# Kernel optimization log

Hardware: AMD Instinct MI355X
Metric: run time of the kernel (lower is better)

## Reference

```python
import jax, jax.numpy as jnp
import numpy as np

NINP = 512
NHEAD = 8


def setup_inputs() -> dict:
    key = jax.random.key(0)
    ks = jax.random.split(key, 7)
    B, M, L, C = 2, 32, 512, NINP
    s = 1.0 / np.sqrt(C)
    return {
        "x": jax.random.normal(ks[0], (B, M, L, C), dtype=jnp.float32),
        "Wq": jax.random.normal(ks[1], (C, C), dtype=jnp.float32) * s,
        "bq": jax.random.normal(ks[2], (C,), dtype=jnp.float32) * s,
        "Wk": jax.random.normal(ks[3], (C, C), dtype=jnp.float32) * s,
        "bk": jax.random.normal(ks[4], (C,), dtype=jnp.float32) * s,
        "Wv": jax.random.normal(ks[5], (C, C), dtype=jnp.float32) * s,
        "bv": jax.random.normal(ks[6], (C,), dtype=jnp.float32) * s,
    }


def reference(x, Wq, bq, Wk, bk, Wv, bv) -> jnp.ndarray:
    # x: (B, M, L, C). Attention over L within each (B, M) block.
    B, M, L, C = x.shape
    H = NHEAD
    D = C // H
    scale = 1.0 / jnp.sqrt(jnp.asarray(D, dtype=x.dtype))

    def split_heads(t):  # (B,M,L,C) -> (B,M,H,L,D)
        return t.reshape(B, M, L, H, D).transpose(0, 1, 3, 2, 4)

    q = split_heads(x @ Wq + bq)
    k = split_heads(x @ Wk + bk)
    v = split_heads(x @ Wv + bv)

    scores = jnp.einsum("bmhid,bmhjd->bmhij", q, k) * scale
    w = jax.nn.softmax(scores, axis=-1)  # dropout p=0 -> identity
    out = jnp.einsum("bmhij,bmhjd->bmhid", w, v)  # (B,M,H,L,D)
    return out.transpose(0, 1, 3, 2, 4).reshape(B, M, L, C)
```

## Files before the change

kernel.cpp:

```cpp
#include <hip/hip_runtime.h>


typedef unsigned short u16;
typedef unsigned int u32;
typedef unsigned long long u64;
typedef __bf16 bf16x8 __attribute__((ext_vector_type(8)));
typedef float f32x4 __attribute__((ext_vector_type(4)));

#define SCQ 0.18033688011112042f

static __device__ __forceinline__ u16 f2bf(float f) {
  u32 x = __float_as_uint(f);
  x += 0x7fffu + ((x >> 16) & 1u);
  return (u16)(x >> 16);
}

static __device__ __forceinline__ u32 pkbf(float f0, float f1) {
  return __builtin_amdgcn_perm(__float_as_uint(f1) + 0x8000u,
                               __float_as_uint(f0) + 0x8000u, 0x07060302u);
}

typedef __attribute__((address_space(1))) const void* gvp;
typedef __attribute__((address_space(3))) void* lvp;
static __device__ __forceinline__ void glds16(const void* g, void* l) {
  __builtin_amdgcn_global_load_lds((gvp)g, (lvp)l, 16, 0, 0);
}

__global__ __launch_bounds__(256) void prep(const float* __restrict__ x,
                                            u16* __restrict__ xb,
                                            const float* __restrict__ Wq,
                                            const float* __restrict__ Wk,
                                            const float* __restrict__ Wv,
                                            u16* __restrict__ WT) {
  __shared__ float t[32][33];
  const int bx = blockIdx.x;
  if (bx < 8192) {
    const u32 i = (bx * 256u + threadIdx.x) * 8u;
    const float4 a = *(const float4*)(x + i);
    const float4 b = *(const float4*)(x + i + 4);
    union { u16 r[8]; uint4 v; } u;
    u.r[0] = f2bf(a.x); u.r[1] = f2bf(a.y); u.r[2] = f2bf(a.z); u.r[3] = f2bf(a.w);
    u.r[4] = f2bf(b.x); u.r[5] = f2bf(b.y); u.r[6] = f2bf(b.z); u.r[7] = f2bf(b.w);
    *(uint4*)(xb + i) = u.v;
    return;
  }
  const int b = bx - 8192;
  const int z = b >> 8;
  const int rem = b & 255;
  const float* W = (z == 0) ? Wq : ((z == 1) ? Wk : Wv);
  u16* dst = WT + z * 262144;
  const int k0 = (rem >> 4) * 32, n0 = (rem & 15) * 32;
  const int tx = threadIdx.x & 31, ty = threadIdx.x >> 5;
#pragma unroll
  for (int i = 0; i < 32; i += 8)
    t[ty + i][tx] = W[(size_t)(k0 + ty + i) * 512 + n0 + tx];
  __syncthreads();
#pragma unroll
  for (int i = 0; i < 32; i += 8)
    dst[(size_t)(n0 + ty + i) * 512 + k0 + tx] = f2bf(t[tx][ty + i]);
}

__global__ __launch_bounds__(256) void gemm_qkv(const u16* __restrict__ xb,
                                                const u16* __restrict__ WT,
                                                const float* __restrict__ bq,
                                                const float* __restrict__ bk,
                                                const float* __restrict__ bv,
                                                u16* __restrict__ qkv) {
  __shared__ __align__(16) u16 smem[24576];
  const int z = blockIdx.z;
  const u16* Bg = WT + z * 262144;
  const float* bias = (z == 0) ? bq : ((z == 1) ? bk : bv);
  u16* out = qkv + (size_t)z * 16777216u;
  const int tid = threadIdx.x;
  const int lane = tid & 63;
  const int w = tid >> 6;
  const int wy = w >> 1, wx = w & 1;
  const int m15 = lane & 15, g = lane >> 4;
  const int mbase = blockIdx.x * 128;
  const int nbase = blockIdx.y * 128;

  const int srow = w * 32 + (lane >> 2);
  const int scol = (lane & 3) * 8;
  const u16* Ap = xb + (size_t)(mbase + srow) * 512 + scol;
  const u16* Bp = Bg + (size_t)(nbase + srow) * 512 + scol;

  f32x4 acc[4][4] = {};

#define STAGE(KT, B)                                  \
  do {                                                \
    const int k0_ = (KT) * 32;                        \
    u16* d_ = (B) + w * 1024;                         \
    glds16(Ap + k0_, d_);                             \
    glds16(Ap + k0_ + 16 * 512, d_ + 512);            \
    glds16(Bp + k0_, d_ + 4096);                      \
    glds16(Bp + k0_ + 16 * 512, d_ + 4096 + 512);     \
  } while (0)

#define COMPUTE(B)                                                          \
  do {                                                                      \
    bf16x8 af[4], bfr[4];                                                   \
    _Pragma("unroll") for (int t = 0; t < 4; ++t)                           \
        af[t] = *(const bf16x8*)&(B)[(wy * 64 + t * 16 + m15) * 32 + g * 8];\
    _Pragma("unroll") for (int t = 0; t < 4; ++t)                           \
        bfr[t] = *(const bf16x8*)&(B)[4096 + (wx * 64 + t * 16 + m15) * 32 + g * 8]; \
    _Pragma("unroll") for (int rt = 0; rt < 4; ++rt)                        \
        _Pragma("unroll") for (int ct = 0; ct < 4; ++ct)                    \
            acc[rt][ct] = __builtin_amdgcn_mfma_f32_16x16x32_bf16(          \
                af[rt], bfr[ct], acc[rt][ct], 0, 0, 0);                     \
  } while (0)

  STAGE(0, smem);
  STAGE(1, smem + 8192);
  STAGE(2, smem + 16384);

#pragma unroll
  for (int kt = 0; kt < 16; ++kt) {
    u16* cb = smem + (kt % 3) * 8192;
    if (kt < 14)
      asm volatile("s_waitcnt vmcnt(8)" ::: "memory");
    else if (kt == 14)
      asm volatile("s_waitcnt vmcnt(4)" ::: "memory");
    else
      asm volatile("s_waitcnt vmcnt(0)" ::: "memory");
    __builtin_amdgcn_s_barrier();
    COMPUTE(cb);
    asm volatile("s_waitcnt lgkmcnt(0)" ::: "memory");
    __builtin_amdgcn_s_barrier();
    if (kt + 3 < 16) STAGE(kt + 3, cb);
  }
#undef STAGE
#undef COMPUTE

  if (z < 2) {
    const float sc = (z == 0) ? SCQ : 1.0f;
#pragma unroll
    for (int ct = 0; ct < 4; ++ct) {
      const int col = nbase + wx * 64 + ct * 16 + m15;
      const float bb = bias[col];
#pragma unroll
      for (int rt = 0; rt < 4; ++rt) {
        const int row0 = mbase + wy * 64 + rt * 16 + g * 4;
#pragma unroll
        for (int r = 0; r < 4; ++r)
          out[(size_t)(row0 + r) * 512 + col] = f2bf((acc[rt][ct][r] + bb) * sc);
      }
    }
  } else {
    const int bm = mbase >> 9, jb = mbase & 511;
    u16* sT = smem;
#pragma unroll
    for (int cn = 0; cn < 4; ++cn) {
      __syncthreads();
      if (wx == (cn >> 1)) {
#pragma unroll
        for (int cte = 0; cte < 2; ++cte) {
          const int ct = (cn & 1) * 2 + cte;
          const int ncol = nbase + wx * 64 + ct * 16 + m15;
          const float bb = bias[ncol];
          const int nl = cte * 16 + m15;
#pragma unroll
          for (int rt = 0; rt < 4; ++rt) {
            u64 pk = 0;
#pragma unroll
            for (int r = 0; r < 4; ++r)
              pk |= (u64)f2bf(acc[rt][ct][r] + bb) << (16 * r);
            *(u64*)&sT[nl * 136 + wy * 64 + rt * 16 + g * 4] = pk;
          }
        }
      }
      __syncthreads();
#pragma unroll
      for (int it = 0; it < 2; ++it) {
        const int nl = it * 16 + (tid >> 4);
        const int ml = (tid & 15) * 8;
        const int ng = nbase + cn * 32 + nl;
        const int h = ng >> 6, d = ng & 63;
        *(uint4*)(out + ((size_t)((bm * 8 + h) * 64 + d)) * 512 + jb + ml) =
            *(const uint4*)&sT[nl * 136 + ml];
      }
    }
  }
}

__global__ __launch_bounds__(256) void attn(const u16* __restrict__ Q,
                                            const u16* __restrict__ K,
                                            const u16* __restrict__ Vt,
                                            float* __restrict__ out) {
  __shared__ __align__(16) char smem[36864];
  u16* sK = (u16*)smem;
  u16* sVT = (u16*)(smem + 9216);
  const int tid = threadIdx.x;
  const int lane = tid & 63;
  const int w = tid >> 6;
  const int m15 = lane & 15, g = lane >> 4;
  const int qt = blockIdx.x, h = blockIdx.y, bm = blockIdx.z;
  const size_t rb = (size_t)bm * 512;
  const int q0 = qt * 128 + w * 32;
  u16* sPT = (u16*)(smem + 18432) + w * 2304;

  bf16x8 qf[2][2];
#pragma unroll
  for (int ct = 0; ct < 2; ++ct)
#pragma unroll
    for (int kc = 0; kc < 2; ++kc)
      qf[ct][kc] =
          *(const bf16x8*)(Q + (rb + q0 + ct * 16 + m15) * 512 + h * 64 + kc * 32 + g * 8);

  f32x4 acc[4][2] = {};
  f32x4 lv[2] = {};

  const int srow = tid >> 3, sc8 = (tid & 7) * 8;
  const u16* Kb = K + rb * 512 + h * 64;
  const u16* Vtb = Vt + (size_t)(bm * 8 + h) * 64 * 512;

  uint4 k0v = *(const uint4*)(Kb + (size_t)srow * 512 + sc8);
  uint4 k1v = *(const uint4*)(Kb + (size_t)(srow + 32) * 512 + sc8);
  uint4 v0v = *(const uint4*)(Vtb + (size_t)srow * 512 + sc8);
  uint4 v1v = *(const uint4*)(Vtb + (size_t)(srow + 32) * 512 + sc8);

  for (int jt = 0; jt < 8; ++jt) {
    asm volatile("s_waitcnt lgkmcnt(0)" ::: "memory");
    __builtin_amdgcn_s_barrier();
    asm volatile("s_waitcnt vmcnt(0)" ::: "memory");
    *(uint4*)&sK[srow * 72 + sc8] = k0v;
    *(uint4*)&sK[(srow + 32) * 72 + sc8] = k1v;
    *(uint4*)&sVT[srow * 72 + sc8] = v0v;
    *(uint4*)&sVT[(srow + 32) * 72 + sc8] = v1v;
    if (jt < 7) {
      const int j1 = (jt + 1) * 64;
      k0v = *(const uint4*)(Kb + (size_t)(j1 + srow) * 512 + sc8);
      k1v = *(const uint4*)(Kb + (size_t)(j1 + srow + 32) * 512 + sc8);
      v0v = *(const uint4*)(Vtb + (size_t)srow * 512 + j1 + sc8);
      v1v = *(const uint4*)(Vtb + (size_t)(srow + 32) * 512 + j1 + sc8);
    }
    asm volatile("s_waitcnt lgkmcnt(0)" ::: "memory");
    __builtin_amdgcn_s_barrier();

    f32x4 s[4][2];
#pragma unroll
    for (int rt = 0; rt < 4; ++rt) {
      const bf16x8 k0 = *(const bf16x8*)&sK[(rt * 16 + m15) * 72 + g * 8];
      const bf16x8 k1 = *(const bf16x8*)&sK[(rt * 16 + m15) * 72 + 32 + g * 8];
#pragma unroll
      for (int ct = 0; ct < 2; ++ct) {
        f32x4 z = {};
        z = __builtin_amdgcn_mfma_f32_16x16x32_bf16(k0, qf[ct][0], z, 0, 0, 0);
        s[rt][ct] = __builtin_amdgcn_mfma_f32_16x16x32_bf16(k1, qf[ct][1], z, 0, 0, 0);
      }
    }

#pragma unroll
    for (int ct = 0; ct < 2; ++ct)
#pragma unroll
      for (int rt = 0; rt < 4; ++rt) {
        f32x4 p;
#pragma unroll
        for (int r = 0; r < 4; ++r) p[r] = exp2f(s[rt][ct][r]);
        lv[ct] += p;
        uint2 pk = {pkbf(p[0], p[1]), pkbf(p[2], p[3])};
        *(uint2*)&sPT[(ct * 16 + m15) * 72 + rt * 16 + g * 4] = pk;
      }

    bf16x8 pb[2][2];
#pragma unroll
    for (int ct = 0; ct < 2; ++ct)
#pragma unroll
      for (int kc = 0; kc < 2; ++kc)
        pb[ct][kc] = *(const bf16x8*)&sPT[(ct * 16 + m15) * 72 + kc * 32 + g * 8];
#pragma unroll
    for (int dt = 0; dt < 4; ++dt) {
      const bf16x8 v0 = *(const bf16x8*)&sVT[(dt * 16 + m15) * 72 + g * 8];
      const bf16x8 v1 = *(const bf16x8*)&sVT[(dt * 16 + m15) * 72 + 32 + g * 8];
#pragma unroll
      for (int ct = 0; ct < 2; ++ct) {
        acc[dt][ct] = __builtin_amdgcn_mfma_f32_16x16x32_bf16(v0, pb[ct][0], acc[dt][ct], 0, 0, 0);
        acc[dt][ct] = __builtin_amdgcn_mfma_f32_16x16x32_bf16(v1, pb[ct][1], acc[dt][ct], 0, 0, 0);
      }
    }
  }

  float inv[2];
#pragma unroll
  for (int ct = 0; ct < 2; ++ct) {
    float l = lv[ct][0] + lv[ct][1] + lv[ct][2] + lv[ct][3];
    l += __shfl_xor(l, 16);
    l += __shfl_xor(l, 32);
    inv[ct] = 1.0f / l;
  }
  __syncthreads();
  float* sO = (float*)(smem + w * 4608);
#pragma unroll
  for (int c = 0; c < 2; ++c) {
#pragma unroll
    for (int dt2 = 0; dt2 < 2; ++dt2)
#pragma unroll
      for (int ct = 0; ct < 2; ++ct) {
        f32x4 v = acc[c * 2 + dt2][ct] * inv[ct];
        *(f32x4*)&sO[(ct * 16 + m15) * 36 + dt2 * 16 + g * 4] = v;
      }
#pragma unroll
    for (int it = 0; it < 4; ++it) {
      const int q = it * 8 + (lane >> 3);
      f32x4 v = *(const f32x4*)&sO[q * 36 + (lane & 7) * 4];
      *(f32x4*)&out[(rb + q0 + q) * 512 + h * 64 + c * 32 + (lane & 7) * 4] = v;
    }
  }
}

extern "C" void kernel_launch(void* const* d_in, const int* in_sizes, int n_in,
                              void* d_out, int out_size, void* d_ws, size_t ws_size,
                              hipStream_t stream) {
  const float* x = (const float*)d_in[0];
  const float* Wq = (const float*)d_in[1];
  const float* bq = (const float*)d_in[2];
  const float* Wk = (const float*)d_in[3];
  const float* bk = (const float*)d_in[4];
  const float* Wv = (const float*)d_in[5];
  const float* bv = (const float*)d_in[6];
  float* out = (float*)d_out;

  u16* ws = (u16*)d_ws;
  u16* xb = ws;
  u16* WT = ws + 16777216;
  u16* qkv = ws + 17563648;

  prep<<<8960, 256, 0, stream>>>(x, xb, Wq, Wk, Wv, WT);
  gemm_qkv<<<dim3(256, 4, 3), 256, 0, stream>>>(xb, WT, bq, bk, bv, qkv);
  attn<<<dim3(4, 8, 64), 256, 0, stream>>>(qkv, qkv + 16777216, qkv + 2 * 16777216, out);
}
```

Before: 269.7 us.

## Load QKV GEMM B operand directly into registers, double-buffer A in LDS

The QKV projection GEMM now fetches the weight (B) fragments straight from global memory into registers in MFMA layout instead of staging them through LDS. Only the activation (A) tiles stay in LDS, double-buffered instead of triple-buffered, which shrinks shared memory from 48KB to 16KB and may allow higher occupancy. The trade-off is less uncoalesced-tolerant global reads for B (each lane reads 16 bytes at strided rows) and a shallower prefetch pipeline, which risks exposing more memory latency. The epilogue's use of smem for the V transpose may also need the buffer size checked.

New measurement: 313.5 us. 1.16x slower.

```diff
diff --git a/kernel.cpp b/kernel.cpp
--- a/kernel.cpp
+++ b/kernel.cpp
@@ -66,7 +66,7 @@
                                                 const float* __restrict__ bk,
                                                 const float* __restrict__ bv,
                                                 u16* __restrict__ qkv) {
-  __shared__ __align__(16) u16 smem[24576];
+  __shared__ __align__(16) u16 smem[8192];
   const int z = blockIdx.z;
   const u16* Bg = WT + z * 262144;
   const float* bias = (z == 0) ? bq : ((z == 1) ? bk : bv);
@@ -82,54 +82,63 @@
   const int srow = w * 32 + (lane >> 2);
   const int scol = (lane & 3) * 8;
   const u16* Ap = xb + (size_t)(mbase + srow) * 512 + scol;
-  const u16* Bp = Bg + (size_t)(nbase + srow) * 512 + scol;
+  const u16* Bf = Bg + (size_t)(nbase + wx * 64 + m15) * 512 + g * 8;
+
+  u16* bufA0 = smem;
+  u16* bufA1 = smem + 4096;
 
   f32x4 acc[4][4] = {};
-
-#define STAGE(KT, B)                                  \
+  bf16x8 breg[2][4];
+
+#define SA(KT, BUF)                                   \
   do {                                                \
     const int k0_ = (KT) * 32;                        \
-    u16* d_ = (B) + w * 1024;                         \
+    u16* d_ = (BUF) + w * 1024;                       \
     glds16(Ap + k0_, d_);                             \
     glds16(Ap + k0_ + 16 * 512, d_ + 512);            \
-    glds16(Bp + k0_, d_ + 4096);                      \
-    glds16(Bp + k0_ + 16 * 512, d_ + 4096 + 512);     \
   } while (0)
 
-#define COMPUTE(B)                                                          \
-  do {                                                                      \
-    bf16x8 af[4], bfr[4];                                                   \
-    _Pragma("unroll") for (int t = 0; t < 4; ++t)                           \
-        af[t] = *(const bf16x8*)&(B)[(wy * 64 + t * 16 + m15) * 32 + g * 8];\
-    _Pragma("unroll") for (int t = 0; t < 4; ++t)                           \
-        bfr[t] = *(const bf16x8*)&(B)[4096 + (wx * 64 + t * 16 + m15) * 32 + g * 8]; \
-    _Pragma("unroll") for (int rt = 0; rt < 4; ++rt)                        \
-        _Pragma("unroll") for (int ct = 0; ct < 4; ++ct)                    \
-            acc[rt][ct] = __builtin_amdgcn_mfma_f32_16x16x32_bf16(          \
-                af[rt], bfr[ct], acc[rt][ct], 0, 0, 0);                     \
+#define BL(KT, IDX)                                                        \
+  do {                                                                     \
+    const int k0_ = (KT) * 32;                                             \
+    _Pragma("unroll") for (int t = 0; t < 4; ++t)                          \
+        breg[IDX][t] = *(const bf16x8*)(Bf + (size_t)t * 16 * 512 + k0_);  \
   } while (0)
 
-  STAGE(0, smem);
-  STAGE(1, smem + 8192);
-  STAGE(2, smem + 16384);
+  SA(0, bufA0);
+  BL(0, 0);
+  SA(1, bufA1);
+  BL(1, 1);
 
 #pragma unroll
   for (int kt = 0; kt < 16; ++kt) {
-    u16* cb = smem + (kt % 3) * 8192;
-    if (kt < 14)
-      asm volatile("s_waitcnt vmcnt(8)" ::: "memory");
-    else if (kt == 14)
-      asm volatile("s_waitcnt vmcnt(4)" ::: "memory");
+    u16* cb = (kt & 1) ? bufA1 : bufA0;
+    if (kt < 15)
+      asm volatile("s_waitcnt vmcnt(6)" ::: "memory");
     else
       asm volatile("s_waitcnt vmcnt(0)" ::: "memory");
     __builtin_amdgcn_s_barrier();
-    COMPUTE(cb);
+    {
+      bf16x8 af[4];
+#pragma unroll
+      for (int t = 0; t < 4; ++t)
+        af[t] = *(const bf16x8*)&cb[(wy * 64 + t * 16 + m15) * 32 + g * 8];
+#pragma unroll
+      for (int rt = 0; rt < 4; ++rt)
+#pragma unroll
+        for (int ct = 0; ct < 4; ++ct)
+          acc[rt][ct] = __builtin_amdgcn_mfma_f32_16x16x32_bf16(
+              af[rt], breg[kt & 1][ct], acc[rt][ct], 0, 0, 0);
+    }
     asm volatile("s_waitcnt lgkmcnt(0)" ::: "memory");
     __builtin_amdgcn_s_barrier();
-    if (kt + 3 < 16) STAGE(kt + 3, cb);
-  }
-#undef STAGE
-#undef COMPUTE
+    if (kt + 2 < 16) {
+      SA(kt + 2, cb);
+      BL(kt + 2, kt & 1);
+    }
+  }
+#undef SA
+#undef BL
 
   if (z < 2) {
     const float sc = (z == 0) ? SCQ : 1.0f;
```
